# Kernel tuning notes

Measured on AMD Instinct MI355X. Metric: run time of the kernel, lower is better.

The kernel has to match this reference:

```python
import jax, jax.numpy as jnp
import numpy as np

V = 30   # len(letter_list)
B = 512  # batch of words
T = 24   # letters per word (incl. start token)


def setup_inputs() -> dict:
    key = jax.random.key(0)
    ks = iter(jax.random.split(key, 32))

    def w(shape, s=0.05):
        return (jax.random.normal(next(ks), shape) * s).astype(jnp.float32)

    return {
        "letters": jax.random.randint(next(ks), (B, T), 0, V),
        "w1_sv": w((750 + V, 250)), "b1_sv": w((250,)),
        "w1_mem": w((750 + V, 500)), "b1_mem": w((500,)),
        "w1_sw": w((750 + V, 500)), "b1_sw": w((500,)),
        "w_sv": w((5, 750, 250)), "b_sv": w((5, 250)),
        "w_mem": w((5, 750, 500)), "b_mem": w((5, 500)),
        "w_sw": w((5, 750, 500)), "b_sw": w((5, 500)),
        "wp1": w((750, 450)), "bp1": w((450,)),
        "wp2": w((450, 300)), "bp2": w((300,)),
        "wp3": w((300, 200)), "bp3": w((200,)),
        "wp4": w((200, 100)), "bp4": w((100,)),
        "wp5": w((100, V)), "bp5": w((V,)),
    }


def reference(letters, w1_sv, b1_sv, w1_mem, b1_mem, w1_sw, b1_sw,
              w_sv, b_sv, w_mem, b_mem, w_sw, b_sw,
              wp1, bp1, wp2, bp2, wp3, bp3, wp4, bp4, wp5, bp5):
    dt = w1_sv.dtype
    Bn = letters.shape[0]
    # [T, B, V] one-hot letter sequence
    onehots = jax.nn.one_hot(letters, V, dtype=dt).transpose(1, 0, 2)

    def gate(xin, wsw, bsw, wm, bm, wsv, bsv, m):
        # switch/mem/statevectform block: s = sigmoid; m = m*s + tanh(mem)*(1-s); x = tanh(sv)
        s = jax.nn.sigmoid(xin @ wsw + bsw)
        m_new = m * s + jnp.tanh(xin @ wm + bm) * (1.0 - s)
        x_new = jnp.tanh(xin @ wsv + bsv)
        return x_new, m_new

    def layer(carry, p):
        # layers 2..6: input is concat(x, m) -> 750
        x, m = carry
        wsv, bsv, wm, bm, wsw, bsw = p
        x, m = gate(jnp.concatenate([x, m], 1), wsw, bsw, wm, bm, wsv, bsv, m)
        return (x, m), None

    def step(carry, k):
        # one_step: layer 1 sees concat(x, m, one_hot) -> 750+V, then 5 stacked layers
        x, m = carry
        x, m = gate(jnp.concatenate([x, m, k], 1), w1_sw, b1_sw, w1_mem, b1_mem, w1_sv, b1_sv, m)
        (x, m), _ = jax.lax.scan(layer, (x, m), (w_sv, b_sv, w_mem, b_mem, w_sw, b_sw))
        return (x, m), None

    x0 = jnp.zeros((Bn, 250), dt)
    m0 = jnp.zeros((Bn, 500), dt)
    (x, m), _ = jax.lax.scan(step, (x0, m0), onehots)

    # predict head
    y = jnp.concatenate([x, m], 1)
    y = jnp.tanh(y @ wp1 + bp1)
    y = jnp.tanh(y @ wp2 + bp2)
    y = jnp.tanh(y @ wp3 + bp3)
    y = jnp.tanh(y @ wp4 + bp4)
    return jax.nn.softmax(y @ wp5 + bp5, axis=1)
```

## Files before the change

### kernel.cpp

```cpp
#include <hip/hip_runtime.h>
#include <math.h>

#define BSZ 512
#define NV 30
#define NT 24
#define SS 768
#define PL (80 * 24 * 512)
#define NBLK 256
#define NSTEP 144

typedef __attribute__((ext_vector_type(8))) short bf16x8;
typedef __attribute__((ext_vector_type(4))) float f32x4;
typedef __attribute__((ext_vector_type(4))) unsigned u32x4;

__device__ __forceinline__ unsigned short f2bf(float f) {
    unsigned u = __float_as_uint(f);
    u += 0x7fffu + ((u >> 16) & 1u);
    return (unsigned short)(u >> 16);
}
__device__ __forceinline__ float bf2f(unsigned short h) {
    return __uint_as_float(((unsigned)h) << 16);
}
__device__ __forceinline__ f32x4 mm(bf16x8 a, bf16x8 b, f32x4 c) {
    return __builtin_amdgcn_mfma_f32_16x16x32_bf16(a, b, c, 0, 0, 0);
}
#define LD8(p) (*(const bf16x8*)(const void*)(p))

__device__ __forceinline__ u32x4 ld16_sc0(const void* p) {
    u32x4 r;
    asm volatile("global_load_dwordx4 %0, %1, off sc0" : "=v"(r) : "v"(p) : "memory");
    return r;
}

struct RecArgs {
    const unsigned short* Pw;
    unsigned* A0; unsigned* A1;
    float* Sfin;
    unsigned int* cnt;
    unsigned int* rel;
    unsigned int* ticket;
    const float* b1_sw; const float* b1_mem; const float* b1_sv;
    const float* b_sw;  const float* b_mem;  const float* b_sv;
    const float* w1_sw; const float* w1_mem; const float* w1_sv;
    const int* letters;
};

__global__ void zero_kernel(float* p, int n) {
    int i = blockIdx.x * blockDim.x + threadIdx.x;
    int st = gridDim.x * blockDim.x;
    for (; i < n; i += st) p[i] = 0.f;
}

__launch_bounds__(64)
__global__ void pack_weights_all(const float* __restrict__ w1_sw, const float* __restrict__ w1_mem,
                                 const float* __restrict__ w1_sv,
                                 const float* __restrict__ w_sw, const float* __restrict__ w_mem,
                                 const float* __restrict__ w_sv,
                                 unsigned short* __restrict__ Pw)
{
    const int kc = blockIdx.x;
    const int nb = blockIdx.y;
    const int lyr = blockIdx.z;
    const int l  = threadIdx.x;
    const int g = l >> 4, c = l & 15;
    const float *Wsw, *Wmem, *Wsv;
    if (lyr == 0) { Wsw = w1_sw; Wmem = w1_mem; Wsv = w1_sv; }
    else {
        Wsw  = w_sw  + (size_t)(lyr - 1) * 750 * 500;
        Wmem = w_mem + (size_t)(lyr - 1) * 750 * 500;
        Wsv  = w_sv  + (size_t)(lyr - 1) * 750 * 250;
    }
    unsigned short* Phi = Pw + (size_t)lyr * 2 * PL;
    unsigned short* Plo = Phi + PL;
    const float* W; int N, nbl;
    if (nb < 32)      { W = Wsw;  N = 500; nbl = nb; }
    else if (nb < 64) { W = Wmem; N = 500; nbl = nb - 32; }
    else              { W = Wsv;  N = 250; nbl = nb - 64; }
    const int n = nbl * 16 + c;
    unsigned short h8[8], l8[8];
    #pragma unroll
    for (int j = 0; j < 8; ++j) {
        const int k = kc * 32 + g * 8 + j;
        const float w = (k < 750 && n < N) ? W[(size_t)k * N + n] : 0.f;
        const unsigned short h = f2bf(w);
        h8[j] = h;
        l8[j] = f2bf(w - bf2f(h));
    }
    const size_t off = ((size_t)nb * 24 + kc) * 512 + (size_t)l * 8;
    #pragma unroll
    for (int j = 0; j < 8; ++j) { Phi[off + j] = h8[j]; Plo[off + j] = l8[j]; }
}

__launch_bounds__(384, 1)
__global__ void recurrence(RecArgs A)
{
    __shared__ __align__(16) unsigned char lds[81920];
    __shared__ int s_j;
    const int tid = threadIdx.x;

    int xcd;
    asm volatile("s_getreg_b32 %0, hwreg(HW_REG_XCC_ID)" : "=s"(xcd));
    xcd &= 7;
    if (tid == 0) s_j = (int)atomicAdd(A.ticket + xcd, 1u);
    __syncthreads();
    const int j = s_j;
    const int quarter = j >> 3, p = j & 7;
    const int m0 = xcd * 64 + quarter * 16;

    const int w  = tid >> 6;
    const int l6 = tid & 63;
    const int g = l6 >> 4, c = l6 & 15;
    const int asw = (c & 7) << 4;

    const int tk = p * 6 + w;
    const bool ispair = (tk < 32);
    const int su = ispair ? tk : (tk - 32);
    const int col = su * 16 + c;

    const size_t lnoff = (size_t)l6 * 8;
    const size_t bofs0 = ((size_t)((ispair ? tk : 64 + su) * 24)) * 512 + lnoff;
    const size_t bofs1 = ((size_t)((32 + tk) * 24)) * 512 + lnoff;

    unsigned* cntw = A.cnt + (xcd << 5);
    unsigned* relw = A.rel + (xcd << 5);

    float mreg[4];
    #pragma unroll
    for (int i = 0; i < 4; ++i) mreg[i] = 0.f;

#define FRAG(pl, kc) (*(const bf16x8*)(lds + (pl) * 24576 + c * 1536 + ((((kc) * 64) + g * 16) ^ asw)))

    #pragma unroll 1
    for (int step = 0; step < NSTEP; ++step) {
        const int tt = step / 6;
        const int l = step - 6 * tt;
        const unsigned* Ain = (step & 1) ? A.A1 : A.A0;
        unsigned* Aout      = (step & 1) ? A.A0 : A.A1;
        const unsigned short* Phi = A.Pw + (size_t)l * 2 * PL;
        const unsigned short* Plo = Phi + PL;
        const bool more = (step != NSTEP - 1);

        {
            const unsigned char* src = (const unsigned char*)(Ain + (size_t)m0 * SS);
            u32x4 tmp[8];
            #pragma unroll
            for (int jj = 0; jj < 8; ++jj) {
                const int f = tid + jj * 384;
                const int row = f / 192;
                const int q = f - row * 192;
                tmp[jj] = ld16_sc0(src + row * 3072 + q * 16);
            }
            asm volatile("s_waitcnt vmcnt(0)" ::: "memory");
            __builtin_amdgcn_sched_barrier(0);
            #pragma unroll
            for (int jj = 0; jj < 8; ++jj) {
                const int f = tid + jj * 384;
                const int row = f / 192;
                const int q = f - row * 192;
                const int d = row * 1536 + ((q * 8) ^ ((row & 7) << 4));
                const u32x4 v = tmp[jj];
                const unsigned h0 = (v[0] & 0xffffu) | (v[1] << 16);
                const unsigned h1 = (v[2] & 0xffffu) | (v[3] << 16);
                const unsigned o0 = (v[0] >> 16) | (v[1] & 0xffff0000u);
                const unsigned o1 = (v[2] >> 16) | (v[3] & 0xffff0000u);
                *(unsigned long long*)(lds + d)         = (unsigned long long)h0 | ((unsigned long long)h1 << 32);
                *(unsigned long long*)(lds + 24576 + d) = (unsigned long long)o0 | ((unsigned long long)o1 << 32);
            }
        }
        __syncthreads();

        if (ispair) {
            f32x4 z0 = (f32x4)0.f, z1 = (f32x4)0.f;
            #pragma unroll
            for (int kc = 0; kc < 24; ++kc) {
                const bf16x8 ah = FRAG(0, kc);
                const bf16x8 al = FRAG(1, kc);
                const size_t k5 = (size_t)kc * 512;
                const bf16x8 bh0 = LD8(Phi + bofs0 + k5);
                const bf16x8 bl0 = LD8(Plo + bofs0 + k5);
                const bf16x8 bh1 = LD8(Phi + bofs1 + k5);
                const bf16x8 bl1 = LD8(Plo + bofs1 + k5);
                z0 = mm(ah, bh0, z0); z0 = mm(al, bh0, z0); z0 = mm(ah, bl0, z0);
                z1 = mm(ah, bh1, z1); z1 = mm(al, bh1, z1); z1 = mm(ah, bl1, z1);
            }
            if (col < 500) {
                const float* bswp  = l ? A.b_sw  + (size_t)(l - 1) * 500 : A.b1_sw;
                const float* bmemp = l ? A.b_mem + (size_t)(l - 1) * 500 : A.b1_mem;
                const float bs = bswp[col];
                const float bm = bmemp[col];
                #pragma unroll
                for (int r = 0; r < 4; ++r) {
                    const int row = m0 + g * 4 + r;
                    float zs = z0[r] + bs;
                    float zm = z1[r] + bm;
                    if (l == 0) {
                        const int lt = A.letters[row * NT + tt];
                        zs += A.w1_sw[(size_t)(750 + lt) * 500 + col];
                        zm += A.w1_mem[(size_t)(750 + lt) * 500 + col];
                    }
                    const float s = 1.f / (1.f + expf(-zs));
                    const float mn = mreg[r] * s + tanhf(zm) * (1.f - s);
                    mreg[r] = mn;
                    const size_t o = (size_t)row * SS + 250 + col;
                    const unsigned short h = f2bf(mn);
                    const unsigned short lo2 = f2bf(mn - bf2f(h));
                    Aout[o] = (unsigned)h | ((unsigned)lo2 << 16);
                    if (step == NSTEP - 1) A.Sfin[o] = mn;
                }
            }
        } else {
            f32x4 z0 = (f32x4)0.f;
            #pragma unroll
            for (int kc = 0; kc < 24; ++kc) {
                const bf16x8 ah = FRAG(0, kc);
                const bf16x8 al = FRAG(1, kc);
                const size_t k5 = (size_t)kc * 512;
                const bf16x8 bh = LD8(Phi + bofs0 + k5);
                const bf16x8 bl = LD8(Plo + bofs0 + k5);
                z0 = mm(ah, bh, z0); z0 = mm(al, bh, z0); z0 = mm(ah, bl, z0);
            }
            if (col < 250) {
                const float* bsvp = l ? A.b_sv + (size_t)(l - 1) * 250 : A.b1_sv;
                const float bv = bsvp[col];
                #pragma unroll
                for (int r = 0; r < 4; ++r) {
                    const int row = m0 + g * 4 + r;
                    float z = z0[r] + bv;
                    if (l == 0) {
                        const int lt = A.letters[row * NT + tt];
                        z += A.w1_sv[(size_t)(750 + lt) * 250 + col];
                    }
                    const float x = tanhf(z);
                    const size_t o = (size_t)row * SS + col;
                    const unsigned short h = f2bf(x);
                    const unsigned short lo2 = f2bf(x - bf2f(h));
                    Aout[o] = (unsigned)h | ((unsigned)lo2 << 16);
                    if (step == NSTEP - 1) A.Sfin[o] = x;
                }
            }
        }

        __syncthreads();
        if (more) {
            if (tid == 0) {
                const unsigned v = __hip_atomic_fetch_add(cntw, 1u, __ATOMIC_RELAXED, __HIP_MEMORY_SCOPE_AGENT);
                if (v == 32u * (unsigned)(step + 1) - 1u) {
                    __hip_atomic_store(relw, (unsigned)(step + 1), __ATOMIC_RELAXED, __HIP_MEMORY_SCOPE_AGENT);
                } else {
                    while (__hip_atomic_load(relw, __ATOMIC_RELAXED, __HIP_MEMORY_SCOPE_AGENT) < (unsigned)(step + 1))
                        __builtin_amdgcn_s_sleep(2);
                }
            }
            __syncthreads();
        }
    }
#undef FRAG
}

__launch_bounds__(128)
__global__ void head_gemm(const float* __restrict__ X, int ldx, int K,
                          const float* __restrict__ W, const float* __restrict__ bias,
                          float* __restrict__ Y, int N)
{
    const int tid = threadIdx.x;
    const int m0 = blockIdx.y * 32;
    const int n0 = blockIdx.x * 64;

    __shared__ float As[2][32][36];
    __shared__ float Bs[2][32][68];

    const int tx = tid & 15, ty = tid >> 4;
    const int kl = tid & 31, rl = tid >> 5;
    const int cl = tid & 63, kg = tid >> 6;
    const bool cok = (n0 + cl) < N;

    float acc[4][4] = {{0.f}};
    float ar[8], br[16];

    {
        const float* a = X + (size_t)(m0 + rl) * ldx + kl;
        #pragma unroll
        for (int i = 0; i < 8; i++) ar[i] = a[(size_t)(4 * i) * ldx];
        #pragma unroll
        for (int i = 0; i < 16; i++)
            br[i] = cok ? W[(size_t)(kg + 2 * i) * N + n0 + cl] : 0.f;
        #pragma unroll
        for (int i = 0; i < 8; i++) As[0][kl][rl + 4 * i] = ar[i];
        #pragma unroll
        for (int i = 0; i < 16; i++) Bs[0][kg + 2 * i][cl] = br[i];
    }
    __syncthreads();

    int buf = 0;
    const int NK = (K + 31) / 32;
    #pragma unroll 1
    for (int kt = 0; kt < NK; kt++) {
        const bool more = (kt + 1 < NK);
        if (more) {
            const int k0 = (kt + 1) * 32;
            const bool ka = (k0 + kl) < K;
            const float* a = X + (size_t)(m0 + rl) * ldx + k0 + kl;
            #pragma unroll
            for (int i = 0; i < 8; i++) ar[i] = ka ? a[(size_t)(4 * i) * ldx] : 0.f;
            #pragma unroll
            for (int i = 0; i < 16; i++) {
                const int kk = k0 + kg + 2 * i;
                br[i] = (cok && kk < K) ? W[(size_t)kk * N + n0 + cl] : 0.f;
            }
        }
        #pragma unroll
        for (int kk = 0; kk < 32; kk++) {
            float4 av = *(const float4*)&As[buf][kk][ty * 4];
            float4 bv = *(const float4*)&Bs[buf][kk][tx * 4];
            const float aa[4] = {av.x, av.y, av.z, av.w};
            const float bb[4] = {bv.x, bv.y, bv.z, bv.w};
            #pragma unroll
            for (int i = 0; i < 4; i++)
                #pragma unroll
                for (int j = 0; j < 4; j++)
                    acc[i][j] = fmaf(aa[i], bb[j], acc[i][j]);
        }
        if (more) {
            #pragma unroll
            for (int i = 0; i < 8; i++) As[buf ^ 1][kl][rl + 4 * i] = ar[i];
            #pragma unroll
            for (int i = 0; i < 16; i++) Bs[buf ^ 1][kg + 2 * i][cl] = br[i];
            __syncthreads();
            buf ^= 1;
        }
    }

    #pragma unroll
    for (int i = 0; i < 4; i++) {
        const int b = m0 + ty * 4 + i;
        #pragma unroll
        for (int j = 0; j < 4; j++) {
            const int n = n0 + tx * 4 + j;
            if (n < N) Y[(size_t)b * N + n] = tanhf(acc[i][j] + bias[n]);
        }
    }
}

__global__ void head_final(const float* __restrict__ Y4, const float* __restrict__ W,
                           const float* __restrict__ bias, float* __restrict__ out)
{
    const int row = blockIdx.x;
    __shared__ float y[100];
    __shared__ float z[NV];
    for (int k = threadIdx.x; k < 100; k += 64) y[k] = Y4[row * 100 + k];
    __syncthreads();
    const int n = threadIdx.x;
    if (n < NV) {
        float acc = bias[n];
        for (int k = 0; k < 100; k++) acc = fmaf(y[k], W[k * NV + n], acc);
        z[n] = acc;
    }
    __syncthreads();
    if (n < NV) {
        float mx = -1e30f;
        for (int i = 0; i < NV; i++) mx = fmaxf(mx, z[i]);
        float sum = 0.f;
        for (int i = 0; i < NV; i++) sum += expf(z[i] - mx);
        out[row * NV + n] = expf(z[n] - mx) / sum;
    }
}

extern "C" void kernel_launch(void* const* d_in, const int* in_sizes, int n_in,
                              void* d_out, int out_size, void* d_ws, size_t ws_size,
                              hipStream_t stream)
{
    const int*   letters = (const int*)  d_in[0];
    const float* w1_sv   = (const float*)d_in[1];
    const float* b1_sv   = (const float*)d_in[2];
    const float* w1_mem  = (const float*)d_in[3];
    const float* b1_mem  = (const float*)d_in[4];
    const float* w1_sw   = (const float*)d_in[5];
    const float* b1_sw   = (const float*)d_in[6];
    const float* w_sv    = (const float*)d_in[7];
    const float* b_sv    = (const float*)d_in[8];
    const float* w_mem   = (const float*)d_in[9];
    const float* b_mem   = (const float*)d_in[10];
    const float* w_sw    = (const float*)d_in[11];
    const float* b_sw    = (const float*)d_in[12];
    const float* wp1 = (const float*)d_in[13]; const float* bp1 = (const float*)d_in[14];
    const float* wp2 = (const float*)d_in[15]; const float* bp2 = (const float*)d_in[16];
    const float* wp3 = (const float*)d_in[17]; const float* bp3 = (const float*)d_in[18];
    const float* wp4 = (const float*)d_in[19]; const float* bp4 = (const float*)d_in[20];
    const float* wp5 = (const float*)d_in[21]; const float* bp5 = (const float*)d_in[22];

    float* Sfin = (float*)d_ws;
    float* cntf = Sfin + (size_t)BSZ * SS;
    unsigned int* cnt = (unsigned int*)cntf;
    unsigned int* rel = cnt + 256;
    unsigned int* ticket = cnt + 512;
    unsigned* A0 = (unsigned*)(cntf + 1024);
    unsigned* A1 = A0 + (size_t)BSZ * SS;
    unsigned short* Pw = (unsigned short*)(A1 + (size_t)BSZ * SS);
    float* Y1 = (float*)(Pw + (size_t)12 * PL);
    float* Y2 = Y1 + (size_t)BSZ * 450;
    float* Y3 = Y2 + (size_t)BSZ * 300;
    float* Y4 = Y3 + (size_t)BSZ * 200;

    zero_kernel<<<512, 256, 0, stream>>>(cntf, 1024 + 2 * BSZ * SS);

    pack_weights_all<<<dim3(24, 80, 6), 64, 0, stream>>>(w1_sw, w1_mem, w1_sv,
                                                         w_sw, w_mem, w_sv, Pw);

    RecArgs ra;
    ra.Pw = Pw;
    ra.A0 = A0; ra.A1 = A1;
    ra.Sfin = Sfin; ra.cnt = cnt; ra.rel = rel; ra.ticket = ticket;
    ra.b1_sw = b1_sw; ra.b1_mem = b1_mem; ra.b1_sv = b1_sv;
    ra.b_sw = b_sw;   ra.b_mem = b_mem;   ra.b_sv = b_sv;
    ra.w1_sw = w1_sw; ra.w1_mem = w1_mem; ra.w1_sv = w1_sv;
    ra.letters = letters;
    recurrence<<<NBLK, 384, 0, stream>>>(ra);

    head_gemm<<<dim3(8, 16), 128, 0, stream>>>(Sfin, SS, 750, wp1, bp1, Y1, 450);
    head_gemm<<<dim3(5, 16), 128, 0, stream>>>(Y1, 450, 450, wp2, bp2, Y2, 300);
    head_gemm<<<dim3(4, 16), 128, 0, stream>>>(Y2, 300, 300, wp3, bp3, Y3, 200);
    head_gemm<<<dim3(2, 16), 128, 0, stream>>>(Y3, 200, 200, wp4, bp4, Y4, 100);
    head_final<<<BSZ, 64, 0, stream>>>(Y4, wp5, bp5, (float*)d_out);
}
```

Before: 2.144 ms.

## Give each recurrence block 32 rows and use per-block flag barrier

Each persistent block now handles two 16-row tiles (32 batch rows), so each weight fragment loaded from global memory feeds twice as many MFMAs. Only 16 of the 32 blocks per XCD do work and the rest exit at once. The atomic-counter barrier is replaced by per-block flags that block 0 polls before it releases the group. This halves redundant weight traffic per step, at the cost of half as many active CUs, a larger LDS footprint and a serialized leader poll.

```diff
diff --git a/kernel.cpp b/kernel.cpp
--- a/kernel.cpp
+++ b/kernel.cpp
@@ -36,7 +36,7 @@
     const unsigned short* Pw;
     unsigned* A0; unsigned* A1;
     float* Sfin;
-    unsigned int* cnt;
+    unsigned int* flags;
     unsigned int* rel;
     unsigned int* ticket;
     const float* b1_sw; const float* b1_mem; const float* b1_sv;
@@ -91,10 +91,10 @@
     for (int j = 0; j < 8; ++j) { Phi[off + j] = h8[j]; Plo[off + j] = l8[j]; }
 }
 
-__launch_bounds__(384, 1)
+__launch_bounds__(384)
 __global__ void recurrence(RecArgs A)
 {
-    __shared__ __align__(16) unsigned char lds[81920];
+    __shared__ __align__(16) unsigned char lds[98304];
     __shared__ int s_j;
     const int tid = threadIdx.x;
 
@@ -104,31 +104,34 @@
     if (tid == 0) s_j = (int)atomicAdd(A.ticket + xcd, 1u);
     __syncthreads();
     const int j = s_j;
-    const int quarter = j >> 3, p = j & 7;
-    const int m0 = xcd * 64 + quarter * 16;
+    if (j >= 16) return;
+    const int rg = j >> 3, p = j & 7;
+    const int m0 = xcd * 64 + rg * 32;
 
     const int w  = tid >> 6;
     const int l6 = tid & 63;
     const int g = l6 >> 4, c = l6 & 15;
     const int asw = (c & 7) << 4;
 
-    const int tk = p * 6 + w;
-    const bool ispair = (tk < 32);
-    const int su = ispair ? tk : (tk - 32);
+    const int cu = p * 6 + w;
+    const bool ispair = (cu < 32);
+    const int su = ispair ? cu : (cu - 32);
     const int col = su * 16 + c;
 
     const size_t lnoff = (size_t)l6 * 8;
-    const size_t bofs0 = ((size_t)((ispair ? tk : 64 + su) * 24)) * 512 + lnoff;
-    const size_t bofs1 = ((size_t)((32 + tk) * 24)) * 512 + lnoff;
-
-    unsigned* cntw = A.cnt + (xcd << 5);
-    unsigned* relw = A.rel + (xcd << 5);
-
-    float mreg[4];
+    const size_t bofs0 = ((size_t)((ispair ? cu : 64 + su) * 24)) * 512 + lnoff;
+    const size_t bofs1 = ((size_t)((32 + cu) * 24)) * 512 + lnoff;
+
+    unsigned* flagw = A.flags + (size_t)xcd * 16 * 32;
+    unsigned* relw  = A.rel + (xcd << 5);
+
+    float mreg[2][4];
     #pragma unroll
-    for (int i = 0; i < 4; ++i) mreg[i] = 0.f;
-
-#define FRAG(pl, kc) (*(const bf16x8*)(lds + (pl) * 24576 + c * 1536 + ((((kc) * 64) + g * 16) ^ asw)))
+    for (int i = 0; i < 2; ++i)
+        #pragma unroll
+        for (int r = 0; r < 4; ++r) mreg[i][r] = 0.f;
+
+#define FRAG(pl, rb, kc) (*(const bf16x8*)(lds + (pl) * 49152 + ((rb) * 16 + c) * 1536 + ((((kc) * 64) + g * 16) ^ asw)))
 
     #pragma unroll 1
     for (int step = 0; step < NSTEP; ++step) {
@@ -142,46 +145,53 @@
 
         {
             const unsigned char* src = (const unsigned char*)(Ain + (size_t)m0 * SS);
-            u32x4 tmp[8];
-            #pragma unroll
-            for (int jj = 0; jj < 8; ++jj) {
-                const int f = tid + jj * 384;
-                const int row = f / 192;
-                const int q = f - row * 192;
-                tmp[jj] = ld16_sc0(src + row * 3072 + q * 16);
-            }
-            asm volatile("s_waitcnt vmcnt(0)" ::: "memory");
-            __builtin_amdgcn_sched_barrier(0);
-            #pragma unroll
-            for (int jj = 0; jj < 8; ++jj) {
-                const int f = tid + jj * 384;
-                const int row = f / 192;
-                const int q = f - row * 192;
-                const int d = row * 1536 + ((q * 8) ^ ((row & 7) << 4));
-                const u32x4 v = tmp[jj];
-                const unsigned h0 = (v[0] & 0xffffu) | (v[1] << 16);
-                const unsigned h1 = (v[2] & 0xffffu) | (v[3] << 16);
-                const unsigned o0 = (v[0] >> 16) | (v[1] & 0xffff0000u);
-                const unsigned o1 = (v[2] >> 16) | (v[3] & 0xffff0000u);
-                *(unsigned long long*)(lds + d)         = (unsigned long long)h0 | ((unsigned long long)h1 << 32);
-                *(unsigned long long*)(lds + 24576 + d) = (unsigned long long)o0 | ((unsigned long long)o1 << 32);
+            #pragma unroll
+            for (int half = 0; half < 2; ++half) {
+                u32x4 tmp[8];
+                #pragma unroll
+                for (int jj = 0; jj < 8; ++jj) {
+                    const int f = tid + (half * 8 + jj) * 384;
+                    const int row = f / 192;
+                    const int q = f - row * 192;
+                    tmp[jj] = ld16_sc0(src + row * 3072 + q * 16);
+                }
+                asm volatile("s_waitcnt vmcnt(0)" ::: "memory");
+                __builtin_amdgcn_sched_barrier(0);
+                #pragma unroll
+                for (int jj = 0; jj < 8; ++jj) {
+                    const int f = tid + (half * 8 + jj) * 384;
+                    const int row = f / 192;
+                    const int q = f - row * 192;
+                    const int d = row * 1536 + ((q * 8) ^ ((row & 7) << 4));
+                    const u32x4 v = tmp[jj];
+                    const unsigned h0 = (v[0] & 0xffffu) | (v[1] << 16);
+                    const unsigned h1 = (v[2] & 0xffffu) | (v[3] << 16);
+                    const unsigned o0 = (v[0] >> 16) | (v[1] & 0xffff0000u);
+                    const unsigned o1 = (v[2] >> 16) | (v[3] & 0xffff0000u);
+                    *(unsigned long long*)(lds + d)         = (unsigned long long)h0 | ((unsigned long long)h1 << 32);
+                    *(unsigned long long*)(lds + 49152 + d) = (unsigned long long)o0 | ((unsigned long long)o1 << 32);
+                }
             }
         }
         __syncthreads();
 
         if (ispair) {
-            f32x4 z0 = (f32x4)0.f, z1 = (f32x4)0.f;
-            #pragma unroll
+            f32x4 z0[2], z1[2];
+            z0[0] = (f32x4)0.f; z0[1] = (f32x4)0.f;
+            z1[0] = (f32x4)0.f; z1[1] = (f32x4)0.f;
+            #pragma unroll 4
             for (int kc = 0; kc < 24; ++kc) {
-                const bf16x8 ah = FRAG(0, kc);
-                const bf16x8 al = FRAG(1, kc);
+                const bf16x8 ah0 = FRAG(0, 0, kc), ah1 = FRAG(0, 1, kc);
+                const bf16x8 al0 = FRAG(1, 0, kc), al1 = FRAG(1, 1, kc);
                 const size_t k5 = (size_t)kc * 512;
                 const bf16x8 bh0 = LD8(Phi + bofs0 + k5);
                 const bf16x8 bl0 = LD8(Plo + bofs0 + k5);
                 const bf16x8 bh1 = LD8(Phi + bofs1 + k5);
                 const bf16x8 bl1 = LD8(Plo + bofs1 + k5);
-                z0 = mm(ah, bh0, z0); z0 = mm(al, bh0, z0); z0 = mm(ah, bl0, z0);
-                z1 = mm(ah, bh1, z1); z1 = mm(al, bh1, z1); z1 = mm(ah, bl1, z1);
+                z0[0] = mm(ah0, bh0, z0[0]); z0[0] = mm(al0, bh0, z0[0]); z0[0] = mm(ah0, bl0, z0[0]);
+                z0[1] = mm(ah1, bh0, z0[1]); z0[1] = mm(al1, bh0, z0[1]); z0[1] = mm(ah1, bl0, z0[1]);
+                z1[0] = mm(ah0, bh1, z1[0]); z1[0] = mm(al0, bh1, z1[0]); z1[0] = mm(ah0, bl1, z1[0]);
+                z1[1] = mm(ah1, bh1, z1[1]); z1[1] = mm(al1, bh1, z1[1]); z1[1] = mm(ah1, bl1, z1[1]);
             }
             if (col < 500) {
                 const float* bswp  = l ? A.b_sw  + (size_t)(l - 1) * 500 : A.b1_sw;
@@ -189,65 +199,83 @@
                 const float bs = bswp[col];
                 const float bm = bmemp[col];
                 #pragma unroll
-                for (int r = 0; r < 4; ++r) {
-                    const int row = m0 + g * 4 + r;
-                    float zs = z0[r] + bs;
-                    float zm = z1[r] + bm;
-                    if (l == 0) {
-                        const int lt = A.letters[row * NT + tt];
-                        zs += A.w1_sw[(size_t)(750 + lt) * 500 + col];
-                        zm += A.w1_mem[(size_t)(750 + lt) * 500 + col];
+                for (int rb = 0; rb < 2; ++rb) {
+                    #pragma unroll
+                    for (int r = 0; r < 4; ++r) {
+                        const int row = m0 + rb * 16 + g * 4 + r;
+                        float zs = z0[rb][r] + bs;
+                        float zm = z1[rb][r] + bm;
+                        if (l == 0) {
+                            const int lt = A.letters[row * NT + tt];
+                            zs += A.w1_sw[(size_t)(750 + lt) * 500 + col];
+                            zm += A.w1_mem[(size_t)(750 + lt) * 500 + col];
+                        }
+                        const float s = 1.f / (1.f + expf(-zs));
+                        const float mn = mreg[rb][r] * s + tanhf(zm) * (1.f - s);
+                        mreg[rb][r] = mn;
+                        const size_t o = (size_t)row * SS + 250 + col;
+                        const unsigned short h = f2bf(mn);
+                        const unsigned short lo2 = f2bf(mn - bf2f(h));
+                        Aout[o] = (unsigned)h | ((unsigned)lo2 << 16);
+                        if (step == NSTEP - 1) A.Sfin[o] = mn;
                     }
-                    const float s = 1.f / (1.f + expf(-zs));
-                    const float mn = mreg[r] * s + tanhf(zm) * (1.f - s);
-                    mreg[r] = mn;
-                    const size_t o = (size_t)row * SS + 250 + col;
-                    const unsigned short h = f2bf(mn);
-                    const unsigned short lo2 = f2bf(mn - bf2f(h));
-                    Aout[o] = (unsigned)h | ((unsigned)lo2 << 16);
-                    if (step == NSTEP - 1) A.Sfin[o] = mn;
                 }
             }
         } else {
-            f32x4 z0 = (f32x4)0.f;
-            #pragma unroll
+            f32x4 z0[2];
+            z0[0] = (f32x4)0.f; z0[1] = (f32x4)0.f;
+            #pragma unroll 4
             for (int kc = 0; kc < 24; ++kc) {
-                const bf16x8 ah = FRAG(0, kc);
-                const bf16x8 al = FRAG(1, kc);
+                const bf16x8 ah0 = FRAG(0, 0, kc), ah1 = FRAG(0, 1, kc);
+                const bf16x8 al0 = FRAG(1, 0, kc), al1 = FRAG(1, 1, kc);
                 const size_t k5 = (size_t)kc * 512;
                 const bf16x8 bh = LD8(Phi + bofs0 + k5);
                 const bf16x8 bl = LD8(Plo + bofs0 + k5);
-                z0 = mm(ah, bh, z0); z0 = mm(al, bh, z0); z0 = mm(ah, bl, z0);
+                z0[0] = mm(ah0, bh, z0[0]); z0[0] = mm(al0, bh, z0[0]); z0[0] = mm(ah0, bl, z0[0]);
+                z0[1] = mm(ah1, bh, z0[1]); z0[1] = mm(al1, bh, z0[1]); z0[1] = mm(ah1, bl, z0[1]);
             }
             if (col < 250) {
                 const float* bsvp = l ? A.b_sv + (size_t)(l - 1) * 250 : A.b1_sv;
                 const float bv = bsvp[col];
                 #pragma unroll
-                for (int r = 0; r < 4; ++r) {
-                    const int row = m0 + g * 4 + r;
-                    float z = z0[r] + bv;
-                    if (l == 0) {
-                        const int lt = A.letters[row * NT + tt];
-                        z += A.w1_sv[(size_t)(750 + lt) * 250 + col];
+                for (int rb = 0; rb < 2; ++rb) {
+                    #pragma unroll
+                    for (int r = 0; r < 4; ++r) {
+                        const int row = m0 + rb * 16 + g * 4 + r;
+                        float z = z0[rb][r] + bv;
+                        if (l == 0) {
+                            const int lt = A.letters[row * NT + tt];
+                            z += A.w1_sv[(size_t)(750 + lt) * 250 + col];
+                        }
+                        const float x = tanhf(z);
+                        const size_t o = (size_t)row * SS + col;
+                        const unsigned short h = f2bf(x);
+                        const unsigned short lo2 = f2bf(x - bf2f(h));
+                        Aout[o] = (unsigned)h | ((unsigned)lo2 << 16);
+                        if (step == NSTEP - 1) A.Sfin[o] = x;
                     }
-                    const float x = tanhf(z);
-                    const size_t o = (size_t)row * SS + col;
-                    const unsigned short h = f2bf(x);
-                    const unsigned short lo2 = f2bf(x - bf2f(h));
-                    Aout[o] = (unsigned)h | ((unsigned)lo2 << 16);
-                    if (step == NSTEP - 1) A.Sfin[o] = x;
                 }
             }
         }
 
         __syncthreads();
         if (more) {
+            const unsigned tgt = (unsigned)(step + 1);
             if (tid == 0) {
-                const unsigned v = __hip_atomic_fetch_add(cntw, 1u, __ATOMIC_RELAXED, __HIP_MEMORY_SCOPE_AGENT);
-                if (v == 32u * (unsigned)(step + 1) - 1u) {
-                    __hip_atomic_store(relw, (unsigned)(step + 1), __ATOMIC_RELAXED, __HIP_MEMORY_SCOPE_AGENT);
+                if (j == 0) {
+                    bool all;
+                    do {
+                        all = true;
+                        #pragma unroll
+                        for (int b = 1; b < 16; ++b)
+                            if (__hip_atomic_load(flagw + b * 32, __ATOMIC_RELAXED, __HIP_MEMORY_SCOPE_AGENT) < tgt)
+                                all = false;
+                        if (!all) __builtin_amdgcn_s_sleep(1);
+                    } while (!all);
+                    __hip_atomic_store(relw, tgt, __ATOMIC_RELAXED, __HIP_MEMORY_SCOPE_AGENT);
                 } else {
-                    while (__hip_atomic_load(relw, __ATOMIC_RELAXED, __HIP_MEMORY_SCOPE_AGENT) < (unsigned)(step + 1))
+                    __hip_atomic_store(flagw + j * 32, tgt, __ATOMIC_RELAXED, __HIP_MEMORY_SCOPE_AGENT);
+                    while (__hip_atomic_load(relw, __ATOMIC_RELAXED, __HIP_MEMORY_SCOPE_AGENT) < tgt)
                         __builtin_amdgcn_s_sleep(2);
                 }
             }
@@ -390,10 +418,10 @@
 
     float* Sfin = (float*)d_ws;
     float* cntf = Sfin + (size_t)BSZ * SS;
-    unsigned int* cnt = (unsigned int*)cntf;
-    unsigned int* rel = cnt + 256;
-    unsigned int* ticket = cnt + 512;
-    unsigned* A0 = (unsigned*)(cntf + 1024);
+    unsigned int* flags  = (unsigned int*)cntf;
+    unsigned int* rel    = flags + 4096;
+    unsigned int* ticket = flags + 4352;
+    unsigned* A0 = (unsigned*)(cntf + 8192);
     unsigned* A1 = A0 + (size_t)BSZ * SS;
     unsigned short* Pw = (unsigned short*)(A1 + (size_t)BSZ * SS);
     float* Y1 = (float*)(Pw + (size_t)12 * PL);
@@ -401,7 +429,7 @@
     float* Y3 = Y2 + (size_t)BSZ * 300;
     float* Y4 = Y3 + (size_t)BSZ * 200;
 
-    zero_kernel<<<512, 256, 0, stream>>>(cntf, 1024 + 2 * BSZ * SS);
+    zero_kernel<<<512, 256, 0, stream>>>(cntf, 8192 + 2 * BSZ * SS);
 
     pack_weights_all<<<dim3(24, 80, 6), 64, 0, stream>>>(w1_sw, w1_mem, w1_sv,
                                                          w_sw, w_mem, w_sv, Pw);
@@ -409,7 +437,7 @@
     RecArgs ra;
     ra.Pw = Pw;
     ra.A0 = A0; ra.A1 = A1;
-    ra.Sfin = Sfin; ra.cnt = cnt; ra.rel = rel; ra.ticket = ticket;
+    ra.Sfin = Sfin; ra.flags = flags; ra.rel = rel; ra.ticket = ticket;
     ra.b1_sw = b1_sw; ra.b1_mem = b1_mem; ra.b1_sv = b1_sv;
     ra.b_sw = b_sw;   ra.b_mem = b_mem;   ra.b_sv = b_sv;
     ra.w1_sw = w1_sw; ra.w1_mem = w1_mem; ra.w1_sv = w1_sv;
```

New measurement: 2.616 ms. 1.22x slower.

## Replace per-XCD atomic step barrier with per-quarter flag barrier

Applied to the files above, without the earlier changes.

Each step barrier now spans only the 8 blocks that share a 16-row batch slice instead of all 32 blocks on an XCD, since rows evolve independently. Arrival uses per-block flag stores polled by a leader block rather than a contended atomic counter, and the leader then publishes a release value. The GEMM k-loops are partially unrolled by 4 instead of fully, and the occupancy hint in the launch bounds is dropped. Both of those may reduce how far ahead global loads are issued. Workspace offsets are enlarged to hold the new flag arrays.

```diff
diff --git a/kernel.cpp b/kernel.cpp
--- a/kernel.cpp
+++ b/kernel.cpp
@@ -36,7 +36,7 @@
     const unsigned short* Pw;
     unsigned* A0; unsigned* A1;
     float* Sfin;
-    unsigned int* cnt;
+    unsigned int* flags;
     unsigned int* rel;
     unsigned int* ticket;
     const float* b1_sw; const float* b1_mem; const float* b1_sv;
@@ -91,7 +91,7 @@
     for (int j = 0; j < 8; ++j) { Phi[off + j] = h8[j]; Plo[off + j] = l8[j]; }
 }
 
-__launch_bounds__(384, 1)
+__launch_bounds__(384)
 __global__ void recurrence(RecArgs A)
 {
     __shared__ __align__(16) unsigned char lds[81920];
@@ -121,8 +121,9 @@
     const size_t bofs0 = ((size_t)((ispair ? tk : 64 + su) * 24)) * 512 + lnoff;
     const size_t bofs1 = ((size_t)((32 + tk) * 24)) * 512 + lnoff;
 
-    unsigned* cntw = A.cnt + (xcd << 5);
-    unsigned* relw = A.rel + (xcd << 5);
+    const int qid = xcd * 4 + quarter;
+    unsigned* flagq = A.flags + (size_t)qid * 8 * 32;
+    unsigned* relq  = A.rel + (size_t)qid * 32;
 
     float mreg[4];
     #pragma unroll
@@ -171,7 +172,7 @@
 
         if (ispair) {
             f32x4 z0 = (f32x4)0.f, z1 = (f32x4)0.f;
-            #pragma unroll
+            #pragma unroll 4
             for (int kc = 0; kc < 24; ++kc) {
                 const bf16x8 ah = FRAG(0, kc);
                 const bf16x8 al = FRAG(1, kc);
@@ -210,7 +211,7 @@
             }
         } else {
             f32x4 z0 = (f32x4)0.f;
-            #pragma unroll
+            #pragma unroll 4
             for (int kc = 0; kc < 24; ++kc) {
                 const bf16x8 ah = FRAG(0, kc);
                 const bf16x8 al = FRAG(1, kc);
@@ -242,12 +243,22 @@
 
         __syncthreads();
         if (more) {
+            const unsigned tgt = (unsigned)(step + 1);
             if (tid == 0) {
-                const unsigned v = __hip_atomic_fetch_add(cntw, 1u, __ATOMIC_RELAXED, __HIP_MEMORY_SCOPE_AGENT);
-                if (v == 32u * (unsigned)(step + 1) - 1u) {
-                    __hip_atomic_store(relw, (unsigned)(step + 1), __ATOMIC_RELAXED, __HIP_MEMORY_SCOPE_AGENT);
+                if (p == 0) {
+                    bool all;
+                    do {
+                        all = true;
+                        #pragma unroll
+                        for (int b = 1; b < 8; ++b)
+                            if (__hip_atomic_load(flagq + b * 32, __ATOMIC_RELAXED, __HIP_MEMORY_SCOPE_AGENT) < tgt)
+                                all = false;
+                        if (!all) __builtin_amdgcn_s_sleep(2);
+                    } while (!all);
+                    __hip_atomic_store(relq, tgt, __ATOMIC_RELAXED, __HIP_MEMORY_SCOPE_AGENT);
                 } else {
-                    while (__hip_atomic_load(relw, __ATOMIC_RELAXED, __HIP_MEMORY_SCOPE_AGENT) < (unsigned)(step + 1))
+                    __hip_atomic_store(flagq + p * 32, tgt, __ATOMIC_RELAXED, __HIP_MEMORY_SCOPE_AGENT);
+                    while (__hip_atomic_load(relq, __ATOMIC_RELAXED, __HIP_MEMORY_SCOPE_AGENT) < tgt)
                         __builtin_amdgcn_s_sleep(2);
                 }
             }
@@ -390,10 +401,10 @@
 
     float* Sfin = (float*)d_ws;
     float* cntf = Sfin + (size_t)BSZ * SS;
-    unsigned int* cnt = (unsigned int*)cntf;
-    unsigned int* rel = cnt + 256;
-    unsigned int* ticket = cnt + 512;
-    unsigned* A0 = (unsigned*)(cntf + 1024);
+    unsigned int* flags  = (unsigned int*)cntf;
+    unsigned int* rel    = flags + 8192;
+    unsigned int* ticket = rel + 1024;
+    unsigned* A0 = (unsigned*)(cntf + 10240);
     unsigned* A1 = A0 + (size_t)BSZ * SS;
     unsigned short* Pw = (unsigned short*)(A1 + (size_t)BSZ * SS);
     float* Y1 = (float*)(Pw + (size_t)12 * PL);
@@ -401,7 +412,7 @@
     float* Y3 = Y2 + (size_t)BSZ * 300;
     float* Y4 = Y3 + (size_t)BSZ * 200;
 
-    zero_kernel<<<512, 256, 0, stream>>>(cntf, 1024 + 2 * BSZ * SS);
+    zero_kernel<<<512, 256, 0, stream>>>(cntf, 10240 + 2 * BSZ * SS);
 
     pack_weights_all<<<dim3(24, 80, 6), 64, 0, stream>>>(w1_sw, w1_mem, w1_sv,
                                                          w_sw, w_mem, w_sv, Pw);
@@ -409,7 +420,7 @@
     RecArgs ra;
     ra.Pw = Pw;
     ra.A0 = A0; ra.A1 = A1;
-    ra.Sfin = Sfin; ra.cnt = cnt; ra.rel = rel; ra.ticket = ticket;
+    ra.Sfin = Sfin; ra.flags = flags; ra.rel = rel; ra.ticket = ticket;
     ra.b1_sw = b1_sw; ra.b1_mem = b1_mem; ra.b1_sv = b1_sv;
     ra.b_sw = b_sw;   ra.b_mem = b_mem;   ra.b_sv = b_sv;
     ra.w1_sw = w1_sw; ra.w1_mem = w1_mem; ra.w1_sv = w1_sv;
```

After: 2.059 ms. -4.0%, faster.
